# Kernel optimization log

Hardware: AMD Instinct MI355X
Metric: run time of the kernel (lower is better)

Reference implementation:

```python
import jax, jax.numpy as jnp
from jax import lax
import numpy as np

N_LEVELS = 200          # triangular mesh resolution -> N = 200*201/2 = 20100 points
T = 4096                # number of applied-field time steps


def _triangle_mesh(n_levels):
    xs = np.linspace(0.0, 1.0, n_levels, dtype=np.float32)
    b, a = np.meshgrid(xs, xs, indexing='ij')
    mask = b <= a  # Preisach triangle: beta <= alpha
    return np.stack([b[mask], a[mask]], axis=-1)  # [N, 2]


def setup_inputs() -> dict:
    key = jax.random.key(0)
    k_h, k_d = jax.random.split(key)
    mesh = jnp.asarray(_triangle_mesh(N_LEVELS))          # [20100, 2]
    n = mesh.shape[0]
    return {
        'h': jax.random.uniform(k_h, (T,), dtype=jnp.float32),   # normalized fields in [0,1]
        'mesh_points': mesh,
        'raw_density': jax.random.normal(k_d, (n,), dtype=jnp.float32),
        'scale': jnp.ones((1,), dtype=jnp.float32),
        'offset': jnp.zeros((1,), dtype=jnp.float32),
    }


def reference(h, mesh_points, raw_density, scale, offset):
    beta = mesh_points[:, 0]   # [N]
    alpha = mesh_points[:, 1]  # [N]
    n = raw_density.shape[0]
    density = jax.nn.softplus(raw_density)  # [N]

    # hs = concat(0, h); previous field for each step
    h_prev = jnp.concatenate([jnp.zeros((1,), h.dtype), h[:-1]])

    one = jnp.asarray(1.0, h.dtype)

    def step(state, hp):
        hi, hpv = hp
        swept_up = jnp.where(alpha <= hi, one, state)    # field increasing
        swept_down = jnp.where(beta >= hi, -one, state)  # field decreasing
        new_state = jnp.where(hi > hpv, swept_up,
                              jnp.where(hi < hpv, swept_down, state))
        return new_state, new_state

    init_state = -jnp.ones((n,), h.dtype)  # negative saturation
    _, states = lax.scan(step, init_state, (h, h_prev))  # [T, N]

    m = states @ density / n  # [T]
    return scale * m + offset  # [T]
```

## Files before the change

kernel.cpp:

```cpp
#include <hip/hip_runtime.h>
#include <math.h>


__device__ __forceinline__ float softplus_f(float x) {
    return fmaxf(x, 0.0f) + log1pf(expf(-fabsf(x)));
}

__global__ __launch_bounds__(256) void build_rows_stats(
    const float* __restrict__ h,
    const float* __restrict__ raw,
    float* __restrict__ Cg,
    float* __restrict__ statg,
    int T, int L, int n, int nrowblocks)
{
    const int W  = L + 1;
    const int SP = (W + 1) & ~1;
    const int nc = (T + 63) >> 6;

    const int lane = threadIdx.x & 63;
    const int wid  = threadIdx.x >> 6;
    const int nwv  = blockDim.x >> 6;

    if ((int)blockIdx.x < nrowblocks) {
        const int j = blockIdx.x * nwv + wid;
        if (j >= L) return;
        float* row = Cg + (size_t)(j + 1) * SP;
        float carry = 0.0f;
        for (int k = 0; 64 * k <= j; ++k) {
            const int i = lane + 64 * k;
            float d = 0.0f;
            if (i <= j) {
                const int p = L * i - (i * (i - 1)) / 2 + (j - i);
                d = softplus_f(raw[p]);
            }
            float x = d;
            for (int o = 1; o < 64; o <<= 1) {
                const float tv = __shfl_up(x, o);
                if (lane >= o) x += tv;
            }
            if (i <= j) row[i + 1] = x + carry;
            carry += __shfl(x, 63);
        }
        const float total = carry;
        for (int b = j + 2 + lane; b <= L; b += 64) row[b] = total;
        if (lane == 0) row[0] = 0.0f;
        if (j == 0) {
            for (int b = lane; b <= L; b += 64) Cg[b] = 0.0f;
        }
    } else {
        const int c = ((int)blockIdx.x - nrowblocks) * nwv + wid;
        if (c >= nc) return;
        const int i = (c << 6) + lane;
        const bool inb = (i < T);
        const float hv = inb ? h[i] : 0.0f;
        const float hp = (inb && i > 0) ? h[i - 1] : 0.0f;
        float mu = (inb && hv > hp) ? hv : -1.0f;
        float md = (inb && hv < hp) ? hv : 2.0f;
        for (int o = 1; o < 64; o <<= 1) {
            mu = fmaxf(mu, __shfl_xor(mu, o));
            md = fminf(md, __shfl_xor(md, o));
        }
        if (lane == 0) { statg[c] = mu; statg[nc + c] = md; }
    }
}

__global__ __launch_bounds__(256) void build_cols(
    float* __restrict__ Cg, int L)
{
    const int W  = L + 1;
    const int SP = (W + 1) & ~1;
    const int lane = threadIdx.x & 63;
    const int b = blockIdx.x * (blockDim.x >> 6) + (threadIdx.x >> 6);
    if (b >= W) return;

    float carry = 0.0f;
    for (int k = 0; k < 4; ++k) {
        const int a = 1 + lane + 64 * k;
        float x = (a <= L) ? Cg[(size_t)a * SP + b] : 0.0f;
        for (int o = 1; o < 64; o <<= 1) {
            const float tv = __shfl_up(x, o);
            if (lane >= o) x += tv;
        }
        if (a <= L) Cg[(size_t)a * SP + b] = x + carry;
        carry += __shfl(x, 63);
    }
}

__global__ __launch_bounds__(256) void hyst_main(
    const float* __restrict__ h,
    const float* __restrict__ mesh,
    const float* __restrict__ Cg,
    const float* __restrict__ statg,
    const float* __restrict__ scale,
    const float* __restrict__ offset,
    float* __restrict__ out,
    int T, int L, int n)
{
    const int W  = L + 1;
    const int SP = (W + 1) & ~1;
    const int nc = (T + 63) >> 6;

    const int lane = threadIdx.x & 63;
    const int wid  = threadIdx.x >> 6;
    const int t = blockIdx.x * (blockDim.x >> 6) + wid;
    if (t >= T) return;

    float xsr[4];
#pragma unroll
    for (int k = 0; k < 4; ++k) {
        const int jj = lane + 64 * k;
        xsr[k] = (jj < L) ? mesh[2 * jj + 1] : 2.0f;
    }

    float u_max = -1.0f, d_min = 2.0f;
    int Acov = 0, Bcov = L;
    int nrec = 0;
    int r_up = 0, r_lo = 0, r_Ap = 0, r_Bp = 0;
    float acc = 0.0f;

    auto flushrec = [&]() {
        if (lane < nrec) {
            float contrib;
            if (r_up) {
                contrib = Cg[r_lo * SP + r_Bp] - Cg[r_Ap * SP + r_Bp];
            } else {
                contrib = -((Cg[L * SP + r_Bp] - Cg[L * SP + r_lo])
                          - (Cg[r_Ap * SP + r_Bp] - Cg[r_Ap * SP + r_lo]));
            }
            acc += contrib;
        }
        nrec = 0;
    };
    auto count_le = [&](float v) -> int {
        return __popcll(__ballot(xsr[0] <= v)) + __popcll(__ballot(xsr[1] <= v))
             + __popcll(__ballot(xsr[2] <= v)) + __popcll(__ballot(xsr[3] <= v));
    };
    auto count_lt = [&](float v) -> int {
        return __popcll(__ballot(xsr[0] < v)) + __popcll(__ballot(xsr[1] < v))
             + __popcll(__ballot(xsr[2] < v)) + __popcll(__ballot(xsr[3] < v));
    };
    auto process_chunk = [&](int c) {
        const int i = (c << 6) + lane;
        const int ic = (i < T) ? i : (T - 1);
        const float hv = h[ic];
        const float hp = (ic > 0) ? h[ic - 1] : 0.0f;
        const bool valid = (i <= t);
        const bool isup = valid && (hv > hp);
        const bool isdn = valid && (hv < hp);
        unsigned long long mup = __ballot(isup && hv > u_max);
        unsigned long long mdn = __ballot(isdn && hv < d_min);
        unsigned long long m = mup | mdn;
        while (m) {
            const int rl = 63 - __builtin_clzll(m);
            const float v = __shfl(hv, rl);
            if ((mup >> rl) & 1ull) {
                u_max = v;
                const int lo = count_le(v);
                if (lo > Acov) {
                    if (lane == nrec) { r_up = 1; r_lo = lo; r_Ap = Acov; r_Bp = Bcov; }
                    ++nrec;
                    Acov = lo;
                    if (nrec == 64) flushrec();
                }
            } else {
                d_min = v;
                const int lo = count_lt(v);
                if (lo < Bcov) {
                    if (lane == nrec) { r_up = 0; r_lo = lo; r_Ap = Acov; r_Bp = Bcov; }
                    ++nrec;
                    Bcov = lo;
                    if (nrec == 64) flushrec();
                }
            }
            const unsigned long long below =
                (rl == 0) ? 0ull : ((1ull << rl) - 1ull);
            mup = __ballot(isup && hv > u_max) & below;
            mdn = __ballot(isdn && hv < d_min) & below;
            m = mup | mdn;
        }
    };

    const int ct = t >> 6;
    process_chunk(ct);

    for (int g = (ct - 1) >> 6; g >= 0; --g) {
        if (Acov >= L || Bcov <= 0) break;
        const int cbase = g << 6;
        const int c = cbase + lane;
        const bool act = (c < ct);
        const float vu = act ? statg[c] : -1.0f;
        const float vd = act ? statg[nc + c] : 2.0f;
        float su = vu, sd = vd;
        for (int o = 1; o < 64; o <<= 1) {
            su = fmaxf(su, __shfl_down(su, o));
            sd = fminf(sd, __shfl_down(sd, o));
        }
        float sue = __shfl_down(su, 1);
        float sde = __shfl_down(sd, 1);
        if (lane == 63) { sue = -1.0f; sde = 2.0f; }
        const bool enter = act && ((vu > fmaxf(u_max, sue)) ||
                                   (vd < fminf(d_min, sde)));
        unsigned long long em = __ballot(enter);
        while (em) {
            const int rl = 63 - __builtin_clzll(em);
            process_chunk(cbase + rl);
            em &= ~(1ull << rl);
            if (Acov >= L || Bcov <= 0) break;
        }
    }

    flushrec();
    if (lane == 0) acc -= Cg[L * SP + Bcov] - Cg[Acov * SP + Bcov];
    for (int o = 1; o < 64; o <<= 1) acc += __shfl_xor(acc, o);
    if (lane == 0) out[t] = scale[0] * (acc / (float)n) + offset[0];
}

extern "C" void kernel_launch(void* const* d_in, const int* in_sizes, int n_in,
                              void* d_out, int out_size, void* d_ws, size_t ws_size,
                              hipStream_t stream) {
    const float* h      = (const float*)d_in[0];
    const float* mesh   = (const float*)d_in[1];
    const float* raw    = (const float*)d_in[2];
    const float* scale  = (const float*)d_in[3];
    const float* offset = (const float*)d_in[4];
    float* out = (float*)d_out;

    const int T = in_sizes[0];
    const int n = in_sizes[2];
    const int L = (int)((sqrt(8.0 * (double)n + 1.0) - 1.0) / 2.0 + 0.5);
    const int W = L + 1;
    const int SP = (W + 1) & ~1;
    const int nc = (T + 63) / 64;

    float* Cg    = (float*)d_ws;
    float* statg = Cg + (size_t)W * SP;

    const int nrowblocks  = (L + 3) / 4;
    const int nstatblocks = (nc + 3) / 4;
    hipLaunchKernelGGL(build_rows_stats, dim3(nrowblocks + nstatblocks),
                       dim3(256), 0, stream, h, raw, Cg, statg, T, L, n,
                       nrowblocks);

    const int ncolblocks = (W + 3) / 4;
    hipLaunchKernelGGL(build_cols, dim3(ncolblocks), dim3(256), 0, stream,
                       Cg, L);

    const int nwv = 4;
    const int grid = (T + nwv - 1) / nwv;
    hipLaunchKernelGGL(hyst_main, dim3(grid), dim3(256), 0, stream,
                       h, mesh, Cg, statg, scale, offset, out, T, L, n);
}
```

Baseline: 26.14 us.

## Fuse table build, stats and hysteresis query into one LDS-resident kernel

Merges the three kernels (row scan plus chunk stats, column scan, per-timestep query) into a single 1024-thread kernel. Each block rebuilds the full 2D prefix-sum density table and the per-chunk max/min stats in shared memory, then answers queries from LDS instead of global memory. This removes two kernel launches and the global-memory round trip of the table. The cost is redundant table construction in every block. The table uses nearly all of the LDS, so only one block fits per CU.

Measured after the change: 64.86 us. +148.1%, slower.

```diff
diff --git a/kernel.cpp b/kernel.cpp
--- a/kernel.cpp
+++ b/kernel.cpp
@@ -6,50 +6,30 @@
     return fmaxf(x, 0.0f) + log1pf(expf(-fabsf(x)));
 }
 
-__global__ __launch_bounds__(256) void build_rows_stats(
+__global__ __launch_bounds__(1024) void hyst_fused(
     const float* __restrict__ h,
+    const float* __restrict__ mesh,
     const float* __restrict__ raw,
-    float* __restrict__ Cg,
-    float* __restrict__ statg,
-    int T, int L, int n, int nrowblocks)
+    const float* __restrict__ scale,
+    const float* __restrict__ offset,
+    float* __restrict__ out,
+    int T, int L, int n)
 {
+    extern __shared__ float smem[];
     const int W  = L + 1;
-    const int SP = (W + 1) & ~1;
+    const int SP = W + 2;
     const int nc = (T + 63) >> 6;
 
-    const int lane = threadIdx.x & 63;
-    const int wid  = threadIdx.x >> 6;
+    float* S     = smem;
+    float* umaxs = smem + W * SP;
+    float* dmins = umaxs + nc;
+
+    const int tid  = threadIdx.x;
+    const int lane = tid & 63;
+    const int wid  = tid >> 6;
     const int nwv  = blockDim.x >> 6;
 
-    if ((int)blockIdx.x < nrowblocks) {
-        const int j = blockIdx.x * nwv + wid;
-        if (j >= L) return;
-        float* row = Cg + (size_t)(j + 1) * SP;
-        float carry = 0.0f;
-        for (int k = 0; 64 * k <= j; ++k) {
-            const int i = lane + 64 * k;
-            float d = 0.0f;
-            if (i <= j) {
-                const int p = L * i - (i * (i - 1)) / 2 + (j - i);
-                d = softplus_f(raw[p]);
-            }
-            float x = d;
-            for (int o = 1; o < 64; o <<= 1) {
-                const float tv = __shfl_up(x, o);
-                if (lane >= o) x += tv;
-            }
-            if (i <= j) row[i + 1] = x + carry;
-            carry += __shfl(x, 63);
-        }
-        const float total = carry;
-        for (int b = j + 2 + lane; b <= L; b += 64) row[b] = total;
-        if (lane == 0) row[0] = 0.0f;
-        if (j == 0) {
-            for (int b = lane; b <= L; b += 64) Cg[b] = 0.0f;
-        }
-    } else {
-        const int c = ((int)blockIdx.x - nrowblocks) * nwv + wid;
-        if (c >= nc) return;
+    for (int c = wid; c < nc; c += nwv) {
         const int i = (c << 6) + lane;
         const bool inb = (i < T);
         const float hv = inb ? h[i] : 0.0f;
@@ -60,50 +40,49 @@
             mu = fmaxf(mu, __shfl_xor(mu, o));
             md = fminf(md, __shfl_xor(md, o));
         }
-        if (lane == 0) { statg[c] = mu; statg[nc + c] = md; }
-    }
-}
-
-__global__ __launch_bounds__(256) void build_cols(
-    float* __restrict__ Cg, int L)
-{
-    const int W  = L + 1;
-    const int SP = (W + 1) & ~1;
-    const int lane = threadIdx.x & 63;
-    const int b = blockIdx.x * (blockDim.x >> 6) + (threadIdx.x >> 6);
-    if (b >= W) return;
-
-    float carry = 0.0f;
-    for (int k = 0; k < 4; ++k) {
-        const int a = 1 + lane + 64 * k;
-        float x = (a <= L) ? Cg[(size_t)a * SP + b] : 0.0f;
-        for (int o = 1; o < 64; o <<= 1) {
-            const float tv = __shfl_up(x, o);
-            if (lane >= o) x += tv;
-        }
-        if (a <= L) Cg[(size_t)a * SP + b] = x + carry;
-        carry += __shfl(x, 63);
-    }
-}
-
-__global__ __launch_bounds__(256) void hyst_main(
-    const float* __restrict__ h,
-    const float* __restrict__ mesh,
-    const float* __restrict__ Cg,
-    const float* __restrict__ statg,
-    const float* __restrict__ scale,
-    const float* __restrict__ offset,
-    float* __restrict__ out,
-    int T, int L, int n)
-{
-    const int W  = L + 1;
-    const int SP = (W + 1) & ~1;
-    const int nc = (T + 63) >> 6;
-
-    const int lane = threadIdx.x & 63;
-    const int wid  = threadIdx.x >> 6;
-    const int t = blockIdx.x * (blockDim.x >> 6) + wid;
-    if (t >= T) return;
+        if (lane == 0) { umaxs[c] = mu; dmins[c] = md; }
+    }
+
+    for (int j = wid; j < L; j += nwv) {
+        float* row = S + (j + 1) * SP;
+        float carry = 0.0f;
+        for (int k = 0; 64 * k <= j; ++k) {
+            const int i = lane + 64 * k;
+            float d = 0.0f;
+            if (i <= j) {
+                const int p = L * i - (i * (i - 1)) / 2 + (j - i);
+                d = softplus_f(raw[p]);
+            }
+            float x = d;
+            for (int o = 1; o < 64; o <<= 1) {
+                const float tv = __shfl_up(x, o);
+                if (lane >= o) x += tv;
+            }
+            if (i <= j) row[i + 1] = x + carry;
+            carry += __shfl(x, 63);
+        }
+        const float total = carry;
+        for (int b = j + 2 + lane; b <= L; b += 64) row[b] = total;
+        if (lane == 0) row[0] = 0.0f;
+    }
+    if (wid == 0) {
+        for (int b = lane; b <= L; b += 64) S[b] = 0.0f;
+    }
+    __syncthreads();
+
+    for (int b = wid; b < W; b += nwv) {
+        float carry = 0.0f;
+        for (int k = 0; 64 * k < L; ++k) {
+            const int a = 1 + lane + 64 * k;
+            float x = (a <= L) ? S[a * SP + b] : 0.0f;
+            for (int o = 1; o < 64; o <<= 1) {
+                const float tv = __shfl_up(x, o);
+                if (lane >= o) x += tv;
+            }
+            if (a <= L) S[a * SP + b] = x + carry;
+            carry += __shfl(x, 63);
+        }
+    }
 
     float xsr[4];
 #pragma unroll
@@ -111,6 +90,10 @@
         const int jj = lane + 64 * k;
         xsr[k] = (jj < L) ? mesh[2 * jj + 1] : 2.0f;
     }
+    __syncthreads();
+
+    const int t = blockIdx.x * nwv + wid;
+    if (t >= T) return;
 
     float u_max = -1.0f, d_min = 2.0f;
     int Acov = 0, Bcov = L;
@@ -122,10 +105,10 @@
         if (lane < nrec) {
             float contrib;
             if (r_up) {
-                contrib = Cg[r_lo * SP + r_Bp] - Cg[r_Ap * SP + r_Bp];
+                contrib = S[r_lo * SP + r_Bp] - S[r_Ap * SP + r_Bp];
             } else {
-                contrib = -((Cg[L * SP + r_Bp] - Cg[L * SP + r_lo])
-                          - (Cg[r_Ap * SP + r_Bp] - Cg[r_Ap * SP + r_lo]));
+                contrib = -((S[L * SP + r_Bp] - S[L * SP + r_lo])
+                          - (S[r_Ap * SP + r_Bp] - S[r_Ap * SP + r_lo]));
             }
             acc += contrib;
         }
@@ -188,8 +171,8 @@
         const int cbase = g << 6;
         const int c = cbase + lane;
         const bool act = (c < ct);
-        const float vu = act ? statg[c] : -1.0f;
-        const float vd = act ? statg[nc + c] : 2.0f;
+        const float vu = act ? umaxs[c] : -1.0f;
+        const float vd = act ? dmins[c] : 2.0f;
         float su = vu, sd = vd;
         for (int o = 1; o < 64; o <<= 1) {
             su = fmaxf(su, __shfl_down(su, o));
@@ -210,7 +193,7 @@
     }
 
     flushrec();
-    if (lane == 0) acc -= Cg[L * SP + Bcov] - Cg[Acov * SP + Bcov];
+    if (lane == 0) acc -= S[L * SP + Bcov] - S[Acov * SP + Bcov];
     for (int o = 1; o < 64; o <<= 1) acc += __shfl_xor(acc, o);
     if (lane == 0) out[t] = scale[0] * (acc / (float)n) + offset[0];
 }
@@ -229,24 +212,16 @@
     const int n = in_sizes[2];
     const int L = (int)((sqrt(8.0 * (double)n + 1.0) - 1.0) / 2.0 + 0.5);
     const int W = L + 1;
-    const int SP = (W + 1) & ~1;
+    const int SP = W + 2;
     const int nc = (T + 63) / 64;
 
-    float* Cg    = (float*)d_ws;
-    float* statg = Cg + (size_t)W * SP;
-
-    const int nrowblocks  = (L + 3) / 4;
-    const int nstatblocks = (nc + 3) / 4;
-    hipLaunchKernelGGL(build_rows_stats, dim3(nrowblocks + nstatblocks),
-                       dim3(256), 0, stream, h, raw, Cg, statg, T, L, n,
-                       nrowblocks);
-
-    const int ncolblocks = (W + 3) / 4;
-    hipLaunchKernelGGL(build_cols, dim3(ncolblocks), dim3(256), 0, stream,
-                       Cg, L);
-
-    const int nwv = 4;
+    const size_t shmem = ((size_t)W * SP + 2 * (size_t)nc) * sizeof(float);
+    (void)hipFuncSetAttribute(reinterpret_cast<const void*>(hyst_fused),
+                              hipFuncAttributeMaxDynamicSharedMemorySize,
+                              (int)shmem);
+
+    const int nwv = 16;
     const int grid = (T + nwv - 1) / nwv;
-    hipLaunchKernelGGL(hyst_main, dim3(grid), dim3(256), 0, stream,
-                       h, mesh, Cg, statg, scale, offset, out, T, L, n);
+    hipLaunchKernelGGL(hyst_fused, dim3(grid), dim3(1024), shmem, stream,
+                       h, mesh, raw, scale, offset, out, T, L, n);
 }
```

## Stage h and chunk stats in LDS; use per-lane serial scans for prefix sums

Applied to the files above, without the earlier changes.

In hyst_main, each block now copies the prefix of h it may need (up to its largest t) and the per-chunk up/down extrema into shared memory before processing, so chunk scans read LDS instead of global memory. The row and column prefix-sum kernels change from a loop of wave scans to a per-lane serial scan of 4 elements followed by a single wave scan. The trade-off is that later blocks copy up to the whole h array even when they only visit a few chunks, which adds global-to-LDS traffic and a barrier. The new scans also assume L fits in 256 entries.

After: 24.89 us. -4.8%, faster.

```diff
diff --git a/kernel.cpp b/kernel.cpp
--- a/kernel.cpp
+++ b/kernel.cpp
@@ -11,7 +11,7 @@
     const float* __restrict__ raw,
     float* __restrict__ Cg,
     float* __restrict__ statg,
-    int T, int L, int n, int nrowblocks)
+    int T, int L, int nrowblocks)
 {
     const int W  = L + 1;
     const int SP = (W + 1) & ~1;
@@ -25,23 +25,30 @@
         const int j = blockIdx.x * nwv + wid;
         if (j >= L) return;
         float* row = Cg + (size_t)(j + 1) * SP;
-        float carry = 0.0f;
-        for (int k = 0; 64 * k <= j; ++k) {
-            const int i = lane + 64 * k;
+        float s[4];
+        float run = 0.0f;
+#pragma unroll
+        for (int q = 0; q < 4; ++q) {
+            const int i = 4 * lane + q;
             float d = 0.0f;
             if (i <= j) {
                 const int p = L * i - (i * (i - 1)) / 2 + (j - i);
                 d = softplus_f(raw[p]);
             }
-            float x = d;
-            for (int o = 1; o < 64; o <<= 1) {
-                const float tv = __shfl_up(x, o);
-                if (lane >= o) x += tv;
-            }
-            if (i <= j) row[i + 1] = x + carry;
-            carry += __shfl(x, 63);
-        }
-        const float total = carry;
+            run += d; s[q] = run;
+        }
+        float x = run;
+        for (int o = 1; o < 64; o <<= 1) {
+            const float tv = __shfl_up(x, o);
+            if (lane >= o) x += tv;
+        }
+        const float excl = x - run;
+#pragma unroll
+        for (int q = 0; q < 4; ++q) {
+            const int i = 4 * lane + q;
+            if (i <= j) row[i + 1] = excl + s[q];
+        }
+        const float total = __shfl(x, 63);
         for (int b = j + 2 + lane; b <= L; b += 64) row[b] = total;
         if (lane == 0) row[0] = 0.0f;
         if (j == 0) {
@@ -73,16 +80,24 @@
     const int b = blockIdx.x * (blockDim.x >> 6) + (threadIdx.x >> 6);
     if (b >= W) return;
 
-    float carry = 0.0f;
-    for (int k = 0; k < 4; ++k) {
-        const int a = 1 + lane + 64 * k;
-        float x = (a <= L) ? Cg[(size_t)a * SP + b] : 0.0f;
-        for (int o = 1; o < 64; o <<= 1) {
-            const float tv = __shfl_up(x, o);
-            if (lane >= o) x += tv;
-        }
-        if (a <= L) Cg[(size_t)a * SP + b] = x + carry;
-        carry += __shfl(x, 63);
+    float v[4];
+    float run = 0.0f;
+#pragma unroll
+    for (int q = 0; q < 4; ++q) {
+        const int a = 1 + 4 * lane + q;
+        const float d = (a <= L) ? Cg[(size_t)a * SP + b] : 0.0f;
+        run += d; v[q] = run;
+    }
+    float x = run;
+    for (int o = 1; o < 64; o <<= 1) {
+        const float tv = __shfl_up(x, o);
+        if (lane >= o) x += tv;
+    }
+    const float excl = x - run;
+#pragma unroll
+    for (int q = 0; q < 4; ++q) {
+        const int a = 1 + 4 * lane + q;
+        if (a <= L) Cg[(size_t)a * SP + b] = excl + v[q];
     }
 }
 
@@ -96,14 +111,29 @@
     float* __restrict__ out,
     int T, int L, int n)
 {
+    extern __shared__ float sm[];
     const int W  = L + 1;
     const int SP = (W + 1) & ~1;
     const int nc = (T + 63) >> 6;
 
-    const int lane = threadIdx.x & 63;
-    const int wid  = threadIdx.x >> 6;
-    const int t = blockIdx.x * (blockDim.x >> 6) + wid;
-    if (t >= T) return;
+    float* lh = sm;
+    float* us = sm + T;
+    float* dsm = us + nc;
+
+    const int tid  = threadIdx.x;
+    const int lane = tid & 63;
+    const int wid  = tid >> 6;
+    const int nwv  = blockDim.x >> 6;
+
+    const int tmax = min(T - 1, (int)(blockIdx.x + 1) * nwv - 1);
+    const int nh4  = (tmax + 4) >> 2;
+    const float4* h4 = (const float4*)h;
+    float4* lh4 = (float4*)lh;
+    for (int k = tid; k < nh4; k += blockDim.x) lh4[k] = h4[k];
+    const int ncb = (tmax >> 6) + 1;
+    for (int k = tid; k < ncb; k += blockDim.x) {
+        us[k] = statg[k]; dsm[k] = statg[nc + k];
+    }
 
     float xsr[4];
 #pragma unroll
@@ -111,6 +141,10 @@
         const int jj = lane + 64 * k;
         xsr[k] = (jj < L) ? mesh[2 * jj + 1] : 2.0f;
     }
+    __syncthreads();
+
+    const int t = blockIdx.x * nwv + wid;
+    if (t >= T) return;
 
     float u_max = -1.0f, d_min = 2.0f;
     int Acov = 0, Bcov = L;
@@ -141,9 +175,8 @@
     };
     auto process_chunk = [&](int c) {
         const int i = (c << 6) + lane;
-        const int ic = (i < T) ? i : (T - 1);
-        const float hv = h[ic];
-        const float hp = (ic > 0) ? h[ic - 1] : 0.0f;
+        const float hv = lh[i];
+        const float hp = (i > 0) ? lh[i - 1] : 0.0f;
         const bool valid = (i <= t);
         const bool isup = valid && (hv > hp);
         const bool isdn = valid && (hv < hp);
@@ -188,8 +221,8 @@
         const int cbase = g << 6;
         const int c = cbase + lane;
         const bool act = (c < ct);
-        const float vu = act ? statg[c] : -1.0f;
-        const float vd = act ? statg[nc + c] : 2.0f;
+        const float vu = act ? us[c] : -1.0f;
+        const float vd = act ? dsm[c] : 2.0f;
         float su = vu, sd = vd;
         for (int o = 1; o < 64; o <<= 1) {
             su = fmaxf(su, __shfl_down(su, o));
@@ -238,7 +271,7 @@
     const int nrowblocks  = (L + 3) / 4;
     const int nstatblocks = (nc + 3) / 4;
     hipLaunchKernelGGL(build_rows_stats, dim3(nrowblocks + nstatblocks),
-                       dim3(256), 0, stream, h, raw, Cg, statg, T, L, n,
+                       dim3(256), 0, stream, h, raw, Cg, statg, T, L,
                        nrowblocks);
 
     const int ncolblocks = (W + 3) / 4;
@@ -247,6 +280,7 @@
 
     const int nwv = 4;
     const int grid = (T + nwv - 1) / nwv;
-    hipLaunchKernelGGL(hyst_main, dim3(grid), dim3(256), 0, stream,
+    const size_t shmem = (size_t)(T + 2 * nc) * sizeof(float);
+    hipLaunchKernelGGL(hyst_main, dim3(grid), dim3(256), shmem, stream,
                        h, mesh, Cg, statg, scale, offset, out, T, L, n);
 }
```
